# Kernel optimization log

Hardware: AMD Instinct MI355X
Metric: run time of the kernel (lower is better)

## Reference

```python
import jax, jax.numpy as jnp
import numpy as np

EMBED_DIM = 1024
HEAD_DIM = 64


def setup_inputs() -> dict:
    key = jax.random.key(0)
    ks = jax.random.split(key, 7)
    B, S = 4, 2048
    s = 1.0 / np.sqrt(EMBED_DIM)
    h = jax.random.normal(ks[0], (B, S, EMBED_DIM), dtype=jnp.float32)
    Wq = jax.random.normal(ks[1], (EMBED_DIM, HEAD_DIM), dtype=jnp.float32) * s
    bq = jax.random.normal(ks[2], (HEAD_DIM,), dtype=jnp.float32) * 0.01
    Wk = jax.random.normal(ks[3], (EMBED_DIM, HEAD_DIM), dtype=jnp.float32) * s
    bk = jax.random.normal(ks[4], (HEAD_DIM,), dtype=jnp.float32) * 0.01
    Wv = jax.random.normal(ks[5], (EMBED_DIM, HEAD_DIM), dtype=jnp.float32) * s
    bv = jax.random.normal(ks[6], (HEAD_DIM,), dtype=jnp.float32) * 0.01
    return {"h": h, "Wq": Wq, "bq": bq, "Wk": Wk, "bk": bk, "Wv": Wv, "bv": bv}


def reference(h, Wq, bq, Wk, bk, Wv, bv):
    # Linear projections: h [B,S,E] -> q,k [B,S,D]
    q = jnp.einsum("bse,ed->bsd", h, Wq) + bq
    k = jnp.einsum("bse,ed->bsd", h, Wk) + bk
    v = jnp.einsum("bse,ed->bsd", h, Wv) + bv  # computed but UNUSED (faithful to source)
    del v
    scale = 1.0 / jnp.sqrt(jnp.asarray(HEAD_DIM, dtype=q.dtype))
    # scores [B, Sq, Sk]
    scores = jnp.einsum("bqd,bkd->bqk", q, k) * scale
    # NOTE: source uses softmax over dim=1 (query axis), not the key axis
    weights = jax.nn.softmax(scores, axis=1)
    # NOTE: source passes h (not v) as the value tensor
    out = jnp.einsum("bqk,bke->bqe", weights, h)  # [B, Sq, E]
    return out
```

## Files before the change

### kernel.cpp

```cpp
#include <hip/hip_runtime.h>
#include <hip/hip_bf16.h>
#include <math.h>

#define EMBED 1024
#define HDIM  64
#define BATCH 4
#define SEQ   2048

typedef __attribute__((ext_vector_type(8))) short short8;
typedef __attribute__((ext_vector_type(4))) float f32x4;
typedef unsigned int u32;
typedef unsigned short u16;

static __device__ __forceinline__ u16 f2bf(float f) {
    union { float f; u32 u; } v; v.f = f;
    u32 r = v.u + 0x7fffu + ((v.u >> 16) & 1u);
    return (u16)(r >> 16);
}
static __device__ __forceinline__ float bf2f(u32 hi16) {
    union { u32 u; float f; } v; v.u = hi16 << 16; return v.f;
}

static __device__ __forceinline__ void gload_lds16(const u16* g, u16* l) {
    __builtin_amdgcn_global_load_lds(
        (const __attribute__((address_space(1))) u32*)g,
        (__attribute__((address_space(3))) u32*)l, 16, 0, 0);
}

__global__ __launch_bounds__(256) void wt_kernel(
    const float* __restrict__ Wq, const float* __restrict__ Wk,
    u16* __restrict__ WqT, u16* __restrict__ WkT)
{
    __shared__ float tile[64][65];
    const float* W = blockIdx.y ? Wk : Wq;
    u16* WT = blockIdx.y ? WkT : WqT;
    int e0 = blockIdx.x * 64;
    int t = threadIdx.x, c = t & 63, r4 = t >> 6;
    for (int r = r4; r < 64; r += 4)
        tile[r][c] = W[(size_t)(e0 + r) * HDIM + c];
    __syncthreads();
    for (int d = r4; d < 64; d += 4)
        WT[(size_t)d * EMBED + e0 + c] = f2bf(tile[c][d]);
}

__global__ __launch_bounds__(256) void proj_kernel(
    const float* __restrict__ h, const u16* __restrict__ WqT, const u16* __restrict__ WkT,
    const float* __restrict__ bq, const float* __restrict__ bk,
    u16* __restrict__ Qbf, u16* __restrict__ Kbf, u16* __restrict__ hT)
{
    __shared__ u16 hs[2][16][72];
    int b = blockIdx.x >> 7, s0 = (blockIdx.x & 127) * 16;
    int t = threadIdx.x, lane = t & 63, w = t >> 6;
    int l15 = lane & 15, quad = lane >> 4;
    int pj = w >> 1, nh = (w & 1) * 32;
    const float* hb = h + ((size_t)b * SEQ + s0) * EMBED;
    u16* hTb = hT + (size_t)b * EMBED * SEQ;
    const u16* Wp = pj ? WkT : WqT;
    int r = t >> 4, c4 = (t & 15) * 4;
    int ej = t >> 2, soff = (t & 3) * 4;

    f32x4 preA = *(const f32x4*)(hb + (size_t)r * EMBED + c4);
    f32x4 preB = *(const f32x4*)(hb + (size_t)r * EMBED + 64 + c4);
    f32x4 accA[2], accB[2];
    accA[0] = accA[1] = accB[0] = accB[1] = (f32x4){0.f, 0.f, 0.f, 0.f};

    const u16* Wrow0 = Wp + (size_t)(nh + l15) * EMBED;
    const u16* Wrow1 = Wp + (size_t)(nh + 16 + l15) * EMBED;

    short8 wf0 = *(const short8*)(Wrow0 + quad * 8);
    short8 wf1 = *(const short8*)(Wrow0 + 32 + quad * 8);
    short8 wf2 = *(const short8*)(Wrow1 + quad * 8);
    short8 wf3 = *(const short8*)(Wrow1 + 32 + quad * 8);

    for (int it = 0; it < 16; ++it) {
        int ec = it * 64, buf = it & 1;
        uint2 pk;
        pk.x = (u32)f2bf(preA[0]) | ((u32)f2bf(preA[1]) << 16);
        pk.y = (u32)f2bf(preA[2]) | ((u32)f2bf(preA[3]) << 16);
        *(uint2*)&hs[buf][r][c4] = pk;
        __syncthreads();
        preA = preB;
        if (it + 2 < 16)
            preB = *(const f32x4*)(hb + (size_t)r * EMBED + ec + 128 + c4);

        short8 nw0 = wf0, nw1 = wf1, nw2 = wf2, nw3 = wf3;
        if (it + 1 < 16) {
            nw0 = *(const short8*)(Wrow0 + ec + 64 + quad * 8);
            nw1 = *(const short8*)(Wrow0 + ec + 96 + quad * 8);
            nw2 = *(const short8*)(Wrow1 + ec + 64 + quad * 8);
            nw3 = *(const short8*)(Wrow1 + ec + 96 + quad * 8);
        }

        {
            u16 v0 = hs[buf][soff    ][ej];
            u16 v1 = hs[buf][soff + 1][ej];
            u16 v2 = hs[buf][soff + 2][ej];
            u16 v3 = hs[buf][soff + 3][ej];
            uint2 pk2;
            pk2.x = (u32)v0 | ((u32)v1 << 16);
            pk2.y = (u32)v2 | ((u32)v3 << 16);
            *(uint2*)(hTb + (size_t)(ec + ej) * SEQ + s0 + soff) = pk2;
        }

        short8 a0 = *(const short8*)&hs[buf][l15][quad * 8];
        short8 a1 = *(const short8*)&hs[buf][l15][32 + quad * 8];
        accA[0] = __builtin_amdgcn_mfma_f32_16x16x32_bf16(a0, wf0, accA[0], 0, 0, 0);
        accA[1] = __builtin_amdgcn_mfma_f32_16x16x32_bf16(a0, wf2, accA[1], 0, 0, 0);
        accB[0] = __builtin_amdgcn_mfma_f32_16x16x32_bf16(a1, wf1, accB[0], 0, 0, 0);
        accB[1] = __builtin_amdgcn_mfma_f32_16x16x32_bf16(a1, wf3, accB[1], 0, 0, 0);
        wf0 = nw0; wf1 = nw1; wf2 = nw2; wf3 = nw3;
    }

    const float* bias = pj ? bk : bq;
    float scale = pj ? 1.0f : 0.125f;
    u16* outp = pj ? Kbf : Qbf;
    float bv0 = bias[nh + l15], bv1 = bias[nh + 16 + l15];
#pragma unroll
    for (int rr = 0; rr < 4; rr++) {
        size_t row = (size_t)b * SEQ + s0 + quad * 4 + rr;
        outp[row * HDIM + nh + l15]      = f2bf((accA[0][rr] + accB[0][rr] + bv0) * scale);
        outp[row * HDIM + nh + 16 + l15] = f2bf((accA[1][rr] + accB[1][rr] + bv1) * scale);
    }
}

__global__ __launch_bounds__(256) void sw_kernel(
    const u16* __restrict__ Qbf, const u16* __restrict__ Kbf,
    u16* __restrict__ Wmat, float* __restrict__ invl)
{
    __shared__ float sl[4][16];
    int b = blockIdx.y;
    int k0 = blockIdx.x * 16;
    int t = threadIdx.x, lane = t & 63, w = t >> 6;
    int l15 = lane & 15, quad = lane >> 4;
    const u16* Qb = Qbf + (size_t)b * SEQ * HDIM;
    const u16* Kb = Kbf + (size_t)b * SEQ * HDIM;
    u16* Wb = Wmat + (size_t)b * SEQ * SEQ;
    short8 kf0 = *(const short8*)(Kb + (size_t)(k0 + l15) * HDIM + quad * 8);
    short8 kf1 = *(const short8*)(Kb + (size_t)(k0 + l15) * HDIM + 32 + quad * 8);
    f32x4 lacc = {0.f, 0.f, 0.f, 0.f};
    int qs = w * 512;
    const u16* qpa = Qb + (size_t)(qs + l15) * HDIM;
    const u16* qpb = Qb + (size_t)(qs + 16 + l15) * HDIM;
    short8 cf0a = *(const short8*)(qpa + quad * 8);
    short8 cf1a = *(const short8*)(qpa + 32 + quad * 8);
    short8 cf0b = *(const short8*)(qpb + quad * 8);
    short8 cf1b = *(const short8*)(qpb + 32 + quad * 8);

    for (int q0 = qs; q0 < qs + 512; q0 += 32) {
        short8 nf0a = cf0a, nf1a = cf1a, nf0b = cf0b, nf1b = cf1b;
        if (q0 + 32 < qs + 512) {
            const u16* na = Qb + (size_t)(q0 + 32 + l15) * HDIM;
            const u16* nb = Qb + (size_t)(q0 + 48 + l15) * HDIM;
            nf0a = *(const short8*)(na + quad * 8);
            nf1a = *(const short8*)(na + 32 + quad * 8);
            nf0b = *(const short8*)(nb + quad * 8);
            nf1b = *(const short8*)(nb + 32 + quad * 8);
        }
        f32x4 aa = {0.f, 0.f, 0.f, 0.f}, ab = {0.f, 0.f, 0.f, 0.f};
        aa = __builtin_amdgcn_mfma_f32_16x16x32_bf16(kf0, cf0a, aa, 0, 0, 0);
        ab = __builtin_amdgcn_mfma_f32_16x16x32_bf16(kf0, cf0b, ab, 0, 0, 0);
        aa = __builtin_amdgcn_mfma_f32_16x16x32_bf16(kf1, cf1a, aa, 0, 0, 0);
        ab = __builtin_amdgcn_mfma_f32_16x16x32_bf16(kf1, cf1b, ab, 0, 0, 0);
        float e0 = __expf(aa[0]), e1 = __expf(aa[1]);
        float e2 = __expf(aa[2]), e3 = __expf(aa[3]);
        float g0 = __expf(ab[0]), g1 = __expf(ab[1]);
        float g2 = __expf(ab[2]), g3 = __expf(ab[3]);
        lacc[0] += e0 + g0; lacc[1] += e1 + g1;
        lacc[2] += e2 + g2; lacc[3] += e3 + g3;
        uint2 pa, pb;
        pa.x = (u32)f2bf(e0) | ((u32)f2bf(e1) << 16);
        pa.y = (u32)f2bf(e2) | ((u32)f2bf(e3) << 16);
        pb.x = (u32)f2bf(g0) | ((u32)f2bf(g1) << 16);
        pb.y = (u32)f2bf(g2) | ((u32)f2bf(g3) << 16);
        *(uint2*)(Wb + (size_t)(q0 + l15) * SEQ + k0 + quad * 4) = pa;
        *(uint2*)(Wb + (size_t)(q0 + 16 + l15) * SEQ + k0 + quad * 4) = pb;
        cf0a = nf0a; cf1a = nf1a; cf0b = nf0b; cf1b = nf1b;
    }
#pragma unroll
    for (int m = 1; m <= 8; m <<= 1) {
        lacc[0] += __shfl_xor(lacc[0], m, 64);
        lacc[1] += __shfl_xor(lacc[1], m, 64);
        lacc[2] += __shfl_xor(lacc[2], m, 64);
        lacc[3] += __shfl_xor(lacc[3], m, 64);
    }
    if (l15 == 0) {
        sl[w][quad * 4 + 0] = lacc[0];
        sl[w][quad * 4 + 1] = lacc[1];
        sl[w][quad * 4 + 2] = lacc[2];
        sl[w][quad * 4 + 3] = lacc[3];
    }
    __syncthreads();
    if (t < 16)
        invl[b * SEQ + k0 + t] =
            1.0f / ((sl[0][t] + sl[1][t]) + (sl[2][t] + sl[3][t]));
}

__global__ __launch_bounds__(256) void hscale_kernel(
    u16* __restrict__ hT, const float* __restrict__ invl)
{
    size_t idx = ((size_t)blockIdx.x * 256 + threadIdx.x) * 8;
    int s = (int)(idx & (SEQ - 1));
    int b = (int)(idx >> 21);
    const float* il = invl + b * SEQ + s;
    f32x4 il0 = *(const f32x4*)(il);
    f32x4 il1 = *(const f32x4*)(il + 4);
    uint4 v = *(const uint4*)(hT + idx);
    u32 wds[4] = {v.x, v.y, v.z, v.w};
    float sc[8] = {il0[0], il0[1], il0[2], il0[3], il1[0], il1[1], il1[2], il1[3]};
#pragma unroll
    for (int i = 0; i < 4; i++) {
        float f0 = bf2f(wds[i] & 0xffffu) * sc[2 * i];
        float f1 = bf2f(wds[i] >> 16) * sc[2 * i + 1];
        wds[i] = (u32)f2bf(f0) | ((u32)f2bf(f1) << 16);
    }
    uint4 o; o.x = wds[0]; o.y = wds[1]; o.z = wds[2]; o.w = wds[3];
    *(uint4*)(hT + idx) = o;
}

__global__ __launch_bounds__(256) void out_gemm_kernel(
    const u16* __restrict__ Wmat, const u16* __restrict__ hT, float* __restrict__ out)
{
    __shared__ u16 As[2][128 * 64];
    __shared__ u16 Bs[2][128 * 64];
    int b = blockIdx.z;
    int q0 = blockIdx.x * 128, e0 = blockIdx.y * 128;
    int t = threadIdx.x, lane = t & 63, w = t >> 6;
    int l15 = lane & 15, quad = lane >> 4;
    const u16* Wb  = Wmat + (size_t)b * SEQ * SEQ;
    const u16* hTb = hT + (size_t)b * EMBED * SEQ;
    int wq = (w & 1) * 64, we = (w >> 1) * 64;

    f32x4 acc[4][4];
#pragma unroll
    for (int qi = 0; qi < 4; qi++)
#pragma unroll
        for (int ei = 0; ei < 4; ei++) acc[qi][ei] = (f32x4){0.f, 0.f, 0.f, 0.f};

    int st_rl = lane >> 3;
    int st_pc = lane & 7;

#define STAGE(bi, k0)                                                          \
    {                                                                          \
        _Pragma("unroll")                                                      \
        for (int ld = 0; ld < 4; ld++) {                                       \
            int rowb = w * 32 + ld * 8;                                        \
            int row  = rowb + st_rl;                                           \
            int cg   = st_pc ^ (row & 7);            \
            gload_lds16(Wb  + (size_t)(q0 + row) * SEQ + (k0) + cg * 8,        \
                        &As[bi][rowb * 64] + lane * 8);                        \
            gload_lds16(hTb + (size_t)(e0 + row) * SEQ + (k0) + cg * 8,        \
                        &Bs[bi][rowb * 64] + lane * 8);                        \
        }                                                                      \
    }

    STAGE(0, 0)

    for (int it = 0; it < 32; ++it) {
        int buf = it & 1;
        __syncthreads();
        if (it + 1 < 32) STAGE(buf ^ 1, (it + 1) * 64)

        short8 af[2][4], bfr[2][4];
#pragma unroll
        for (int kf = 0; kf < 2; kf++)
#pragma unroll
            for (int i = 0; i < 4; i++) {
                int ra = wq + i * 16 + l15;
                int rb = we + i * 16 + l15;
                int pca = (kf * 4 + quad) ^ (ra & 7);
                int pcb = (kf * 4 + quad) ^ (rb & 7);
                af[kf][i]  = *(const short8*)(&As[buf][ra * 64] + pca * 8);
                bfr[kf][i] = *(const short8*)(&Bs[buf][rb * 64] + pcb * 8);
            }
#pragma unroll
        for (int kf = 0; kf < 2; kf++)
#pragma unroll
            for (int qi = 0; qi < 4; qi++)
#pragma unroll
                for (int ei = 0; ei < 4; ei++)
                    acc[qi][ei] = __builtin_amdgcn_mfma_f32_16x16x32_bf16(
                        af[kf][qi], bfr[kf][ei], acc[qi][ei], 0, 0, 0);
    }
#undef STAGE

    float* outb = out + (size_t)b * SEQ * EMBED;
#pragma unroll
    for (int qi = 0; qi < 4; qi++)
#pragma unroll
        for (int ei = 0; ei < 4; ei++)
#pragma unroll
            for (int r = 0; r < 4; r++)
                outb[(size_t)(q0 + wq + qi * 16 + quad * 4 + r) * EMBED
                     + e0 + we + ei * 16 + l15] = acc[qi][ei][r];
}

extern "C" void kernel_launch(void* const* d_in, const int* in_sizes, int n_in,
                              void* d_out, int out_size, void* d_ws, size_t ws_size,
                              hipStream_t stream) {
    (void)in_sizes; (void)n_in; (void)out_size; (void)ws_size;
    const float* h  = (const float*)d_in[0];
    const float* Wq = (const float*)d_in[1];
    const float* bq = (const float*)d_in[2];
    const float* Wk = (const float*)d_in[3];
    const float* bk = (const float*)d_in[4];
    float* out = (float*)d_out;

    char* ws = (char*)d_ws;
    u16*   Qbf  = (u16*)(ws);
    u16*   Kbf  = (u16*)(ws + (1ull << 20));
    u16*   hT   = (u16*)(ws + (2ull << 20));
    float* invl = (float*)(ws + (18ull << 20));
    u16*   WqT  = (u16*)(ws + (18ull << 20) + (128ull << 10));
    u16*   WkT  = (u16*)(ws + (18ull << 20) + (256ull << 10));
    u16*   Wmat = (u16*)(ws + (19ull << 20));

    hipLaunchKernelGGL(wt_kernel, dim3(16, 2), dim3(256), 0, stream, Wq, Wk, WqT, WkT);
    hipLaunchKernelGGL(proj_kernel, dim3(512), dim3(256), 0, stream,
                       h, WqT, WkT, bq, bk, Qbf, Kbf, hT);
    hipLaunchKernelGGL(sw_kernel, dim3(128, 4), dim3(256), 0, stream,
                       Qbf, Kbf, Wmat, invl);
    hipLaunchKernelGGL(hscale_kernel, dim3(4096), dim3(256), 0, stream, hT, invl);
    hipLaunchKernelGGL(out_gemm_kernel, dim3(16, 8, 4), dim3(256), 0, stream,
                       Wmat, hT, out);
}
```

Baseline: 203.7 us.

## Move h transpose out of projection into fused transpose-scale kernel

The projection kernel no longer writes the transposed bf16 h. It now processes 128 embedding columns per iteration with 8 MFMAs instead of 4, halving the loop trips and barriers. A new tscale_kernel reads fp32 h directly, transposes it through shared memory, multiplies by the inverse softmax denominators and writes bf16 hT in one pass. This replaces the separate read-modify-write hscale pass, at the cost of re-reading the fp32 h (32 MB) and doing uncoalesced 2-byte stores in the transpose.

```diff
diff --git a/kernel.cpp b/kernel.cpp
--- a/kernel.cpp
+++ b/kernel.cpp
@@ -16,9 +16,6 @@
     union { float f; u32 u; } v; v.f = f;
     u32 r = v.u + 0x7fffu + ((v.u >> 16) & 1u);
     return (u16)(r >> 16);
-}
-static __device__ __forceinline__ float bf2f(u32 hi16) {
-    union { u32 u; float f; } v; v.u = hi16 << 16; return v.f;
 }
 
 static __device__ __forceinline__ void gload_lds16(const u16* g, u16* l) {
@@ -46,69 +43,72 @@
 __global__ __launch_bounds__(256) void proj_kernel(
     const float* __restrict__ h, const u16* __restrict__ WqT, const u16* __restrict__ WkT,
     const float* __restrict__ bq, const float* __restrict__ bk,
-    u16* __restrict__ Qbf, u16* __restrict__ Kbf, u16* __restrict__ hT)
-{
-    __shared__ u16 hs[2][16][72];
+    u16* __restrict__ Qbf, u16* __restrict__ Kbf)
+{
+    __shared__ u16 hs[2][16][136];
     int b = blockIdx.x >> 7, s0 = (blockIdx.x & 127) * 16;
     int t = threadIdx.x, lane = t & 63, w = t >> 6;
     int l15 = lane & 15, quad = lane >> 4;
     int pj = w >> 1, nh = (w & 1) * 32;
     const float* hb = h + ((size_t)b * SEQ + s0) * EMBED;
-    u16* hTb = hT + (size_t)b * EMBED * SEQ;
     const u16* Wp = pj ? WkT : WqT;
     int r = t >> 4, c4 = (t & 15) * 4;
-    int ej = t >> 2, soff = (t & 3) * 4;
-
-    f32x4 preA = *(const f32x4*)(hb + (size_t)r * EMBED + c4);
-    f32x4 preB = *(const f32x4*)(hb + (size_t)r * EMBED + 64 + c4);
+
+    f32x4 pre0 = *(const f32x4*)(hb + (size_t)r * EMBED + c4);
+    f32x4 pre1 = *(const f32x4*)(hb + (size_t)r * EMBED + 64 + c4);
     f32x4 accA[2], accB[2];
     accA[0] = accA[1] = accB[0] = accB[1] = (f32x4){0.f, 0.f, 0.f, 0.f};
 
     const u16* Wrow0 = Wp + (size_t)(nh + l15) * EMBED;
     const u16* Wrow1 = Wp + (size_t)(nh + 16 + l15) * EMBED;
 
-    short8 wf0 = *(const short8*)(Wrow0 + quad * 8);
-    short8 wf1 = *(const short8*)(Wrow0 + 32 + quad * 8);
-    short8 wf2 = *(const short8*)(Wrow1 + quad * 8);
-    short8 wf3 = *(const short8*)(Wrow1 + 32 + quad * 8);
-
-    for (int it = 0; it < 16; ++it) {
-        int ec = it * 64, buf = it & 1;
+    short8 cw[8];
+#pragma unroll
+    for (int i = 0; i < 4; i++) {
+        cw[i]     = *(const short8*)(Wrow0 + i * 32 + quad * 8);
+        cw[4 + i] = *(const short8*)(Wrow1 + i * 32 + quad * 8);
+    }
+
+    for (int it = 0; it < 8; ++it) {
+        int ec = it * 128, buf = it & 1;
         uint2 pk;
-        pk.x = (u32)f2bf(preA[0]) | ((u32)f2bf(preA[1]) << 16);
-        pk.y = (u32)f2bf(preA[2]) | ((u32)f2bf(preA[3]) << 16);
+        pk.x = (u32)f2bf(pre0[0]) | ((u32)f2bf(pre0[1]) << 16);
+        pk.y = (u32)f2bf(pre0[2]) | ((u32)f2bf(pre0[3]) << 16);
         *(uint2*)&hs[buf][r][c4] = pk;
+        pk.x = (u32)f2bf(pre1[0]) | ((u32)f2bf(pre1[1]) << 16);
+        pk.y = (u32)f2bf(pre1[2]) | ((u32)f2bf(pre1[3]) << 16);
+        *(uint2*)&hs[buf][r][64 + c4] = pk;
         __syncthreads();
-        preA = preB;
-        if (it + 2 < 16)
-            preB = *(const f32x4*)(hb + (size_t)r * EMBED + ec + 128 + c4);
-
-        short8 nw0 = wf0, nw1 = wf1, nw2 = wf2, nw3 = wf3;
-        if (it + 1 < 16) {
-            nw0 = *(const short8*)(Wrow0 + ec + 64 + quad * 8);
-            nw1 = *(const short8*)(Wrow0 + ec + 96 + quad * 8);
-            nw2 = *(const short8*)(Wrow1 + ec + 64 + quad * 8);
-            nw3 = *(const short8*)(Wrow1 + ec + 96 + quad * 8);
+
+        if (it + 1 < 8) {
+            pre0 = *(const f32x4*)(hb + (size_t)r * EMBED + ec + 128 + c4);
+            pre1 = *(const f32x4*)(hb + (size_t)r * EMBED + ec + 192 + c4);
         }
-
-        {
-            u16 v0 = hs[buf][soff    ][ej];
-            u16 v1 = hs[buf][soff + 1][ej];
-            u16 v2 = hs[buf][soff + 2][ej];
-            u16 v3 = hs[buf][soff + 3][ej];
-            uint2 pk2;
-            pk2.x = (u32)v0 | ((u32)v1 << 16);
-            pk2.y = (u32)v2 | ((u32)v3 << 16);
-            *(uint2*)(hTb + (size_t)(ec + ej) * SEQ + s0 + soff) = pk2;
+        short8 nw[8];
+#pragma unroll
+        for (int i = 0; i < 8; i++) nw[i] = cw[i];
+        if (it + 1 < 8) {
+#pragma unroll
+            for (int i = 0; i < 4; i++) {
+                nw[i]     = *(const short8*)(Wrow0 + ec + 128 + i * 32 + quad * 8);
+                nw[4 + i] = *(const short8*)(Wrow1 + ec + 128 + i * 32 + quad * 8);
+            }
         }
 
         short8 a0 = *(const short8*)&hs[buf][l15][quad * 8];
         short8 a1 = *(const short8*)&hs[buf][l15][32 + quad * 8];
-        accA[0] = __builtin_amdgcn_mfma_f32_16x16x32_bf16(a0, wf0, accA[0], 0, 0, 0);
-        accA[1] = __builtin_amdgcn_mfma_f32_16x16x32_bf16(a0, wf2, accA[1], 0, 0, 0);
-        accB[0] = __builtin_amdgcn_mfma_f32_16x16x32_bf16(a1, wf1, accB[0], 0, 0, 0);
-        accB[1] = __builtin_amdgcn_mfma_f32_16x16x32_bf16(a1, wf3, accB[1], 0, 0, 0);
-        wf0 = nw0; wf1 = nw1; wf2 = nw2; wf3 = nw3;
+        short8 a2 = *(const short8*)&hs[buf][l15][64 + quad * 8];
+        short8 a3 = *(const short8*)&hs[buf][l15][96 + quad * 8];
+        accA[0] = __builtin_amdgcn_mfma_f32_16x16x32_bf16(a0, cw[0], accA[0], 0, 0, 0);
+        accA[1] = __builtin_amdgcn_mfma_f32_16x16x32_bf16(a0, cw[4], accA[1], 0, 0, 0);
+        accB[0] = __builtin_amdgcn_mfma_f32_16x16x32_bf16(a1, cw[1], accB[0], 0, 0, 0);
+        accB[1] = __builtin_amdgcn_mfma_f32_16x16x32_bf16(a1, cw[5], accB[1], 0, 0, 0);
+        accA[0] = __builtin_amdgcn_mfma_f32_16x16x32_bf16(a2, cw[2], accA[0], 0, 0, 0);
+        accA[1] = __builtin_amdgcn_mfma_f32_16x16x32_bf16(a2, cw[6], accA[1], 0, 0, 0);
+        accB[0] = __builtin_amdgcn_mfma_f32_16x16x32_bf16(a3, cw[3], accB[0], 0, 0, 0);
+        accB[1] = __builtin_amdgcn_mfma_f32_16x16x32_bf16(a3, cw[7], accB[1], 0, 0, 0);
+#pragma unroll
+        for (int i = 0; i < 8; i++) cw[i] = nw[i];
     }
 
     const float* bias = pj ? bk : bq;
@@ -195,26 +195,22 @@
             1.0f / ((sl[0][t] + sl[1][t]) + (sl[2][t] + sl[3][t]));
 }
 
-__global__ __launch_bounds__(256) void hscale_kernel(
-    u16* __restrict__ hT, const float* __restrict__ invl)
-{
-    size_t idx = ((size_t)blockIdx.x * 256 + threadIdx.x) * 8;
-    int s = (int)(idx & (SEQ - 1));
-    int b = (int)(idx >> 21);
-    const float* il = invl + b * SEQ + s;
-    f32x4 il0 = *(const f32x4*)(il);
-    f32x4 il1 = *(const f32x4*)(il + 4);
-    uint4 v = *(const uint4*)(hT + idx);
-    u32 wds[4] = {v.x, v.y, v.z, v.w};
-    float sc[8] = {il0[0], il0[1], il0[2], il0[3], il1[0], il1[1], il1[2], il1[3]};
-#pragma unroll
-    for (int i = 0; i < 4; i++) {
-        float f0 = bf2f(wds[i] & 0xffffu) * sc[2 * i];
-        float f1 = bf2f(wds[i] >> 16) * sc[2 * i + 1];
-        wds[i] = (u32)f2bf(f0) | ((u32)f2bf(f1) << 16);
-    }
-    uint4 o; o.x = wds[0]; o.y = wds[1]; o.z = wds[2]; o.w = wds[3];
-    *(uint4*)(hT + idx) = o;
+__global__ __launch_bounds__(256) void tscale_kernel(
+    const float* __restrict__ h, const float* __restrict__ invl,
+    u16* __restrict__ hT)
+{
+    __shared__ float tile[64][65];
+    int b  = blockIdx.z;
+    int s0 = blockIdx.x * 64, e0 = blockIdx.y * 64;
+    int t = threadIdx.x, c = t & 63, r4 = t >> 6;
+    const float* hb = h + (size_t)b * SEQ * EMBED;
+    for (int r = r4; r < 64; r += 4)
+        tile[r][c] = hb[(size_t)(s0 + r) * EMBED + e0 + c];
+    __syncthreads();
+    float il = invl[b * SEQ + s0 + c];
+    u16* hTb = hT + (size_t)b * EMBED * SEQ;
+    for (int er = r4; er < 64; er += 4)
+        hTb[(size_t)(e0 + er) * SEQ + s0 + c] = f2bf(tile[c][er] * il);
 }
 
 __global__ __launch_bounds__(256) void out_gemm_kernel(
@@ -316,10 +312,11 @@
 
     hipLaunchKernelGGL(wt_kernel, dim3(16, 2), dim3(256), 0, stream, Wq, Wk, WqT, WkT);
     hipLaunchKernelGGL(proj_kernel, dim3(512), dim3(256), 0, stream,
-                       h, WqT, WkT, bq, bk, Qbf, Kbf, hT);
+                       h, WqT, WkT, bq, bk, Qbf, Kbf);
     hipLaunchKernelGGL(sw_kernel, dim3(128, 4), dim3(256), 0, stream,
                        Qbf, Kbf, Wmat, invl);
-    hipLaunchKernelGGL(hscale_kernel, dim3(4096), dim3(256), 0, stream, hT, invl);
+    hipLaunchKernelGGL(tscale_kernel, dim3(32, 16, 4), dim3(256), 0, stream,
+                       h, invl, hT);
     hipLaunchKernelGGL(out_gemm_kernel, dim3(16, 8, 4), dim3(256), 0, stream,
                        Wmat, hT, out);
 }
```

Result: faster. 192.0 us (-5.8%).
